# Optimization experiments

Hardware: AMD Instinct MI355X
Metric: run time of the kernel (lower is better)

## Reference

```python
import jax, jax.numpy as jnp
import numpy as np

N, CIN, T, V = 32, 64, 256, 25
COUT = 192
K = 3                      # num_subset
INTER = COUT // 4          # coff_embedding = 4 -> 48
MID = COUT // 3            # 64
EPS = 1e-5


def _bn(x, g, b):
    # training-mode BatchNorm2d over (N, T, V) per channel
    m = x.mean(axis=(0, 2, 3), keepdims=True)
    v = x.var(axis=(0, 2, 3), keepdims=True)
    return (x - m) * jax.lax.rsqrt(v + EPS) * g[None, :, None, None] + b[None, :, None, None]


def _conv1x1(x, w, b):
    # w: [O, C]
    return jnp.einsum('oc,nctv->notv', w, x) + b[None, :, None, None]


def _tconv(x, w, b, pad):
    # w: [O, C, k, 1] temporal conv along T
    y = jax.lax.conv_general_dilated(x, w, (1, 1), ((pad, pad), (0, 0)),
                                     dimension_numbers=('NCHW', 'OIHW', 'NCHW'))
    return y + b[None, :, None, None]


def setup_inputs() -> dict:
    key = jax.random.key(0)
    ks = jax.random.split(key, 24)
    r = lambda i, shape, s=0.05: jax.random.normal(ks[i], shape, jnp.float32) * s
    return {
        'x': r(0, (N, CIN, T, V), 1.0),
        'A': jax.random.uniform(ks[1], (K, V, V), jnp.float32),   # fixed adjacency buffer
        'PA': jnp.full((K, V, V), 1e-6, jnp.float32),
        'Wa': r(2, (K, INTER, CIN)), 'ba': jnp.zeros((K, INTER), jnp.float32),
        'Wb': r(3, (K, INTER, CIN)), 'bb': jnp.zeros((K, INTER), jnp.float32),
        'Wd': r(4, (K, COUT, CIN)), 'bd': jnp.zeros((K, COUT), jnp.float32),
        'gcn_bn_g': jnp.ones(COUT, jnp.float32), 'gcn_bn_b': jnp.zeros(COUT, jnp.float32),
        'down_w': r(5, (COUT, CIN)), 'down_b': jnp.zeros(COUT, jnp.float32),
        'down_bn_g': jnp.ones(COUT, jnp.float32), 'down_bn_b': jnp.zeros(COUT, jnp.float32),
        'W11': r(6, (COUT, COUT)), 'b11': jnp.zeros(COUT, jnp.float32),
        'W21': r(7, (COUT, COUT)), 'b21': jnp.zeros(COUT, jnp.float32),
        'W31': r(8, (COUT, COUT)), 'b31': jnp.zeros(COUT, jnp.float32),
        'W12': r(9, (MID, COUT, 1, 1)), 'b12': jnp.zeros(MID, jnp.float32),
        'W22': r(10, (MID, COUT, 3, 1)), 'b22': jnp.zeros(MID, jnp.float32),
        'W32': r(11, (MID, COUT, 7, 1)), 'b32': jnp.zeros(MID, jnp.float32),
        'tcn_bn_g': jnp.ones(COUT, jnp.float32), 'tcn_bn_b': jnp.zeros(COUT, jnp.float32),
        'res_w': r(12, (COUT, CIN)), 'res_b': jnp.zeros(COUT, jnp.float32),
        'res_bn_g': jnp.ones(COUT, jnp.float32), 'res_bn_b': jnp.zeros(COUT, jnp.float32),
    }


def reference(x, A, PA, Wa, ba, Wb, bb, Wd, bd, gcn_bn_g, gcn_bn_b,
              down_w, down_b, down_bn_g, down_bn_b,
              W11, b11, W21, b21, W31, b31, W12, b12, W22, b22, W32, b32,
              tcn_bn_g, tcn_bn_b, res_w, res_b, res_bn_g, res_bn_b):
    n, c, t, v = x.shape
    # ---- unit_gcn (all num_subset branches vectorized over axis k) ----
    fa = jnp.einsum('kic,nctv->nkitv', Wa, x) + ba[None, :, :, None, None]
    fb = jnp.einsum('kic,nctv->nkitv', Wb, x) + bb[None, :, :, None, None]
    A1 = fa.transpose(0, 1, 4, 2, 3).reshape(n, K, v, INTER * t)   # [n,k,V,inter*T]
    A2 = fb.reshape(n, K, INTER * t, v)                            # [n,k,inter*T,V]
    scores = jnp.einsum('nkvd,nkdw->nkvw', A1, A2) / A1.shape[-1]
    att = jax.nn.softmax(scores, axis=-2) + (A + PA)[None]         # softmax over rows (dim -2)
    xv = x.reshape(n, c * t, v)
    z = jnp.einsum('ndv,nkvw->nkdw', xv, att).reshape(n, K, c, t, v)
    y = jnp.einsum('koc,nkctv->notv', Wd, z) + bd.sum(axis=0)[None, :, None, None]
    y = _bn(y, gcn_bn_g, gcn_bn_b)
    y = y + _bn(_conv1x1(x, down_w, down_b), down_bn_g, down_bn_b)
    g = jax.nn.relu(y)
    # ---- unit_tcn_m: three parallel (1x1 conv -> temporal conv) branches ----
    x1 = _tconv(_conv1x1(g, W11, b11), W12, b12, 0)
    x2 = _tconv(_conv1x1(g, W21, b21), W22, b22, 1)
    x3 = _tconv(_conv1x1(g, W31, b31), W32, b32, 3)
    tm = _bn(jnp.concatenate([x1, x2, x3], axis=1), tcn_bn_g, tcn_bn_b)
    # ---- residual: 1x1 unit_tcn on original input ----
    res = _bn(_conv1x1(x, res_w, res_b), res_bn_g, res_bn_b)
    return jax.nn.relu(tm + res)
```

## Files before the change

kernel.cpp:

```cpp
#include <hip/hip_runtime.h>
#include <hip/hip_bf16.h>
#include <cstdint>
#include <cstddef>

#define EPS_  1e-5f
#define NTV_  204800

typedef unsigned short u16;
typedef __attribute__((ext_vector_type(8))) short short8;
typedef __attribute__((ext_vector_type(4))) float f32x4;

__device__ __forceinline__ float bf2f(u16 u) {
  uint32_t x = (uint32_t)u << 16;
  float f;
  __builtin_memcpy(&f, &x, 4);
  return f;
}
__device__ __forceinline__ u16 f2bf(float f) {
  uint32_t x;
  __builtin_memcpy(&x, &f, 4);
  uint32_t r = (x + 0x7FFFu + ((x >> 16) & 1u)) >> 16;
  return (u16)r;
}

__device__ __forceinline__ void gload_lds16(const u16* g, u16* l) {
  __builtin_amdgcn_global_load_lds(
      (const __attribute__((address_space(1))) uint32_t*)g,
      (__attribute__((address_space(3))) uint32_t*)l, 16, 0, 0);
}

__global__ __launch_bounds__(256) void k_cvtw(
    const float* __restrict__ Wa, const float* __restrict__ Wb_,
    const float* __restrict__ dw, const float* __restrict__ rw,
    const float* __restrict__ W11, const float* __restrict__ W21, const float* __restrict__ W31,
    const float* __restrict__ Wd, const float* __restrict__ W12, const float* __restrict__ W22,
    const float* __restrict__ W32, const float* __restrict__ bd,
    const float* __restrict__ ba, const float* __restrict__ bb,
    const float* __restrict__ downbi, const float* __restrict__ resbi,
    const float* __restrict__ b11, const float* __restrict__ b21, const float* __restrict__ b31,
    u16* __restrict__ WB, float* __restrict__ bd2, float* __restrict__ fbias,
    float* __restrict__ cbias)
{
  int i = blockIdx.x * 256 + threadIdx.x;
  if (i < 9216) { WB[i] = f2bf(Wa[i]); return; }
  i -= 9216;
  if (i < 9216) { WB[9216 + i] = f2bf(Wb_[i]); return; }
  i -= 9216;
  if (i < 12288) { WB[18432 + i] = f2bf(dw[i]); return; }
  i -= 12288;
  if (i < 12288) { WB[30720 + i] = f2bf(rw[i]); return; }
  i -= 12288;
  if (i < 36864) { WB[43008 + i] = f2bf(W11[i]); return; }
  i -= 36864;
  if (i < 36864) { WB[79872 + i] = f2bf(W21[i]); return; }
  i -= 36864;
  if (i < 36864) { WB[116736 + i] = f2bf(W31[i]); return; }
  i -= 36864;
  if (i < 36864) {
    const int o = i / 192, r = i % 192, k = r >> 6, c = r & 63;
    WB[153600 + i] = f2bf(Wd[((size_t)(k * 192 + o)) * 64 + c]);
    return;
  }
  i -= 36864;
  if (i < 12288) { WB[190464 + i] = f2bf(W12[i]); return; }
  i -= 12288;
  if (i < 36864) {
    const int tap = i / 12288, q = i % 12288, o = q / 192, c = q % 192;
    WB[202752 + i] = f2bf(W22[((size_t)(o * 192 + c)) * 3 + tap]);
    return;
  }
  i -= 36864;
  if (i < 86016) {
    const int tap = i / 12288, q = i % 12288, o = q / 192, c = q % 192;
    WB[239616 + i] = f2bf(W32[((size_t)(o * 192 + c)) * 7 + tap]);
    return;
  }
  i -= 86016;
  if (i < 192) { bd2[i] = bd[i] + bd[192 + i] + bd[384 + i]; return; }
  i -= 192;
  if (i < 288) { fbias[i] = (i < 144) ? ba[i] : bb[i - 144]; return; }
  i -= 288;
  if (i < 960) {
    const int g = i / 192, o = i % 192;
    float v;
    if (g == 0) v = downbi[o];
    else if (g == 1) v = resbi[o];
    else if (g == 2) v = b11[o];
    else if (g == 3) v = b21[o];
    else v = b31[o];
    cbias[i] = v;
  }
}

__global__ __launch_bounds__(256) void k_xpose(const float* __restrict__ x, u16* __restrict__ xb)
{
  __shared__ u16 xt[256][72];
  const int bx = blockIdx.x;
  const int n = bx / 25, s0 = (bx % 25) * 256;
  const int tid = threadIdx.x;
  for (int l = tid; l < 64 * 64; l += 256) {
    const int c = l >> 6, q = l & 63;
    float4 v = *(const float4*)&x[((size_t)n * 64 + c) * 6400 + s0 + q * 4];
    xt[q * 4 + 0][c] = f2bf(v.x);
    xt[q * 4 + 1][c] = f2bf(v.y);
    xt[q * 4 + 2][c] = f2bf(v.z);
    xt[q * 4 + 3][c] = f2bf(v.w);
  }
  __syncthreads();
  for (int l = tid; l < 256 * 8; l += 256) {
    const int row = l >> 3, seg = l & 7;
    const int s_old = s0 + row;
    const int dv = s_old % 25, dt = s_old / 25;
    *(uint4*)&xb[((size_t)n * 6400 + dv * 256 + dt) * 64 + seg * 8] = *(const uint4*)&xt[row][seg * 8];
  }
}

template<int C, int NP, bool STATS>
__global__ __launch_bounds__(192) void k_conv5(
    const u16* __restrict__ in, const u16* __restrict__ Wb,
    const float* __restrict__ bias,
    u16* __restrict__ out0, u16* __restrict__ out1, u16* __restrict__ out2,
    float* __restrict__ stSum, float* __restrict__ stSq)
{
  constexpr int CS = C / 8;
  constexpr int CH = C / 32;
  constexpr int SB = 128 * CS;
  __shared__ u16 Bt[128 * C];
  __shared__ u16 Ep[3][16 * 72];

  const int bx = blockIdx.x;
  const int nb = bx / 50;
  const int sb = (bx % 50) * 128;
  const int tid = threadIdx.x;
  const int w = tid >> 6, lane = tid & 63;
  const int lr = lane & 15, lg = lane >> 4;

  for (int base = 0; base < SB; base += 192) {
    const int slot = base + tid;
    if ((SB % 192 == 0) || slot < SB) {
      const int r = slot / CS, q = slot % CS;
      gload_lds16(&in[((size_t)nb * 6400 + sb + r) * C + ((q ^ (r & 7)) << 3)],
                  &Bt[(size_t)(base + w * 64) * 8]);
    }
  }
  __syncthreads();

  u16* sc = Ep[w];
  const int o_w = w * 64;
  const int s0 = lane >> 3, seg = lane & 7;

  for (int p = 0; p < NP; ++p) {
    u16* outp = (p == 0) ? out0 : ((p == 1) ? out1 : out2);
    const u16* Ap = Wb + (size_t)p * 192 * C;
    short8 af[4][CH];
#pragma unroll
    for (int mi = 0; mi < 4; ++mi)
#pragma unroll
      for (int j = 0; j < CH; ++j)
        af[mi][j] = *(const short8*)&Ap[((size_t)(o_w + mi * 16 + lr)) * C + j * 32 + lg * 8];
    float4 bv[4];
#pragma unroll
    for (int mi = 0; mi < 4; ++mi)
      bv[mi] = *(const float4*)&bias[p * 192 + o_w + mi * 16 + lg * 4];
    float ssum[4][4] = {}, ssq[4][4] = {};

#pragma unroll
    for (int t = 0; t < 8; ++t) {
      f32x4 acc[4];
#pragma unroll
      for (int mi = 0; mi < 4; ++mi) {
        acc[mi][0] = 0.f; acc[mi][1] = 0.f; acc[mi][2] = 0.f; acc[mi][3] = 0.f;
      }
      const int rr = t * 16 + lr;
#pragma unroll
      for (int j = 0; j < CH; ++j) {
        short8 bf = *(const short8*)&Bt[((size_t)rr * CS + ((j * 4 + lg) ^ (rr & 7))) * 8];
#pragma unroll
        for (int mi = 0; mi < 4; ++mi)
          acc[mi] = __builtin_amdgcn_mfma_f32_16x16x32_bf16(af[mi][j], bf, acc[mi], 0, 0, 0);
      }
#pragma unroll
      for (int mi = 0; mi < 4; ++mi)
#pragma unroll
        for (int r = 0; r < 4; ++r) {
          float vv = acc[mi][r] + ((const float*)&bv[mi])[r];
          if (STATS) { ssum[mi][r] += vv; ssq[mi][r] += vv * vv; }
          sc[lr * 72 + mi * 16 + lg * 4 + r] = f2bf(vv);
        }
#pragma unroll
      for (int pass = 0; pass < 2; ++pass) {
        const int s = pass * 8 + s0;
        uint4 val = *(const uint4*)&sc[s * 72 + seg * 8];
        *(uint4*)&outp[((size_t)nb * 6400 + sb + t * 16 + s) * 192 + o_w + seg * 8] = val;
      }
    }

    if (STATS) {
#pragma unroll
      for (int mi = 0; mi < 4; ++mi)
#pragma unroll
        for (int r = 0; r < 4; ++r) {
          float ss = ssum[mi][r], sq = ssq[mi][r];
#pragma unroll
          for (int m = 1; m < 16; m <<= 1) { ss += __shfl_xor(ss, m); sq += __shfl_xor(sq, m); }
          if (lr == 0) {
            const int og = p * 192 + o_w + mi * 16 + lg * 4 + r;
            const int slot = bx & 15;
            atomicAdd(&stSum[og * 16 + slot], ss);
            atomicAdd(&stSq[og * 16 + slot], sq);
          }
        }
    }
  }
}

template<int KT>
__global__ __launch_bounds__(256, 2) void k_tconv4(
    const u16* __restrict__ in, const u16* __restrict__ Wb,
    const float* __restrict__ bias, u16* __restrict__ out,
    float* __restrict__ stSum, float* __restrict__ stSq,
    const u16* __restrict__ zp, int o_off)
{
  constexpr int C = 192, CS = 24, CH = 6;
  constexpr int HALO = KT / 2;
  constexpr int BR = 128 + 2 * HALO;
  __shared__ u16 Bt[BR * C];
  __shared__ u16 Ep[4][16 * 24];

  const int bx = blockIdx.x;
  const int nb = bx / 50;
  const int sb = (bx % 50) * 128;
  const int tbase = sb & 255;
  const int tid = threadIdx.x;
  const int w = tid >> 6, lane = tid & 63;
  const int lr = lane & 15, lg = lane >> 4;

  constexpr int SB = BR * CS;
  for (int base = 0; base < SB; base += 256) {
    const int slot = base + tid;
    if ((SB % 256 == 0) || slot < SB) {
      const int r = slot / CS, q = slot % CS;
      const int t = tbase - HALO + r;
      const u16* src = (HALO == 0 || (unsigned)t < 256u)
          ? &in[((size_t)nb * 6400 + sb - HALO + r) * C + ((q ^ (r & 7)) << 3)]
          : zp;
      gload_lds16(src, &Bt[(size_t)(base + w * 64) * 8]);
    }
  }
  __syncthreads();

  f32x4 acc[8];
#pragma unroll
  for (int t = 0; t < 8; ++t) {
    acc[t][0] = 0.f; acc[t][1] = 0.f; acc[t][2] = 0.f; acc[t][3] = 0.f;
  }

  for (int tap = 0; tap < KT; ++tap) {
    short8 af[CH];
#pragma unroll
    for (int j = 0; j < CH; ++j)
      af[j] = *(const short8*)&Wb[((size_t)(tap * 64 + w * 16 + lr)) * C + j * 32 + lg * 8];
#pragma unroll
    for (int t = 0; t < 8; ++t) {
      const int rr = t * 16 + lr + tap;
#pragma unroll
      for (int j = 0; j < CH; ++j) {
        short8 bf = *(const short8*)&Bt[((size_t)rr * CS + ((j * 4 + lg) ^ (rr & 7))) * 8];
        acc[t] = __builtin_amdgcn_mfma_f32_16x16x32_bf16(af[j], bf, acc[t], 0, 0, 0);
      }
    }
  }

  const float4 bv4 = *(const float4*)&bias[w * 16 + lg * 4];
  const int row2 = lane >> 2, q2 = lane & 3;
  float ssum[4] = {}, ssq[4] = {};
#pragma unroll
  for (int t = 0; t < 8; ++t) {
    u16* sc = Ep[w];
#pragma unroll
    for (int r = 0; r < 4; ++r) {
      float vv = acc[t][r] + ((const float*)&bv4)[r];
      ssum[r] += vv; ssq[r] += vv * vv;
      sc[lr * 24 + lg * 4 + r] = f2bf(vv);
    }
    uint2 val = *(const uint2*)&sc[row2 * 24 + q2 * 4];
    *(uint2*)&out[((size_t)nb * 6400 + sb + t * 16 + row2) * 192 +
                  o_off + w * 16 + q2 * 4] = val;
  }
#pragma unroll
  for (int r = 0; r < 4; ++r) {
    float ss = ssum[r], sq = ssq[r];
#pragma unroll
    for (int m = 1; m < 16; m <<= 1) { ss += __shfl_xor(ss, m); sq += __shfl_xor(sq, m); }
    if (lr == 0) {
      const int og = o_off + w * 16 + lg * 4 + r;
      const int slot = bx & 15;
      atomicAdd(&stSum[og * 16 + slot], ss);
      atomicAdd(&stSq[og * 16 + slot], sq);
    }
  }
}

__global__ __launch_bounds__(256) void k_gemm_cf(
    const u16* __restrict__ in, const u16* __restrict__ Wb,
    const float* __restrict__ bias, u16* __restrict__ out)
{
  __shared__ u16 Bt[128 * 64];
  __shared__ u16 At[288 * 64];
  __shared__ u16 SC[48 * 136];

  const int bx = blockIdx.x;
  const int nb = bx / 50;
  const int sb = (bx % 50) * 128;
  const int v = sb >> 8, tbase = sb & 255;
  const int tid = threadIdx.x;
  const int w = tid >> 6, lane = tid & 63;
  const int lr = lane & 15, lg = lane >> 4;
  const int s_w = w * 32;

  for (int base = 0; base < 1024; base += 256) {
    const int slot = base + tid;
    const int r = slot >> 3, q = slot & 7;
    gload_lds16(&in[((size_t)nb * 6400 + v * 256 + tbase + r) * 64 + ((q ^ (r & 7)) << 3)],
                &Bt[(size_t)(base + w * 64) * 8]);
  }
  for (int base = 0; base < 2304; base += 256) {
    const int slot = base + tid;
    const int r = slot >> 3, q = slot & 7;
    gload_lds16(&Wb[(size_t)r * 64 + ((q ^ (r & 7)) << 3)],
                &At[(size_t)(base + w * 64) * 8]);
  }
  __syncthreads();

  for (int p = 0; p < 6; ++p) {
    f32x4 acc[3][2];
#pragma unroll
    for (int mi = 0; mi < 3; ++mi)
#pragma unroll
      for (int ni = 0; ni < 2; ++ni) {
        acc[mi][ni][0] = 0.f; acc[mi][ni][1] = 0.f; acc[mi][ni][2] = 0.f; acc[mi][ni][3] = 0.f;
      }
#pragma unroll
    for (int ch = 0; ch < 2; ++ch) {
      const int j = ch * 4 + lg;
      short8 af[3], bf[2];
#pragma unroll
      for (int mi = 0; mi < 3; ++mi) {
        const int r = p * 48 + mi * 16 + lr;
        af[mi] = *(const short8*)&At[((size_t)r * 8 + (j ^ (r & 7))) * 8];
      }
#pragma unroll
      for (int ni = 0; ni < 2; ++ni) {
        const int r = s_w + ni * 16 + lr;
        bf[ni] = *(const short8*)&Bt[((size_t)r * 8 + (j ^ (r & 7))) * 8];
      }
#pragma unroll
      for (int mi = 0; mi < 3; ++mi)
#pragma unroll
        for (int ni = 0; ni < 2; ++ni)
          acc[mi][ni] = __builtin_amdgcn_mfma_f32_16x16x32_bf16(af[mi], bf[ni], acc[mi][ni], 0, 0, 0);
    }
#pragma unroll
    for (int mi = 0; mi < 3; ++mi)
#pragma unroll
      for (int r = 0; r < 4; ++r) {
        const float bv = bias[p * 48 + mi * 16 + lg * 4 + r];
#pragma unroll
        for (int ni = 0; ni < 2; ++ni) acc[mi][ni][r] += bv;
      }
    __syncthreads();
#pragma unroll
    for (int mi = 0; mi < 3; ++mi)
#pragma unroll
      for (int ni = 0; ni < 2; ++ni)
#pragma unroll
        for (int r = 0; r < 4; ++r)
          SC[(mi * 16 + lg * 4 + r) * 136 + s_w + ni * 16 + lr] = f2bf(acc[mi][ni][r]);
    __syncthreads();
#pragma unroll
    for (int it = 0; it < 3; ++it) {
      const int row = it * 16 + (tid >> 4), chunk = tid & 15;
      *(uint4*)&out[((size_t)nb * 288 + p * 48 + row) * 6400 + sb + chunk * 8] =
          *(const uint4*)&SC[row * 136 + chunk * 8];
    }
  }
}

__device__ __forceinline__ float dot4(uint2 a, uint2 b) {
  return bf2f((u16)(a.x & 0xffff)) * bf2f((u16)(b.x & 0xffff)) +
         bf2f((u16)(a.x >> 16))    * bf2f((u16)(b.x >> 16)) +
         bf2f((u16)(a.y & 0xffff)) * bf2f((u16)(b.y & 0xffff)) +
         bf2f((u16)(a.y >> 16))    * bf2f((u16)(b.y >> 16));
}

__global__ __launch_bounds__(256) void k_scores_part(
    const u16* __restrict__ fab, float* __restrict__ part)
{
  const int nk = blockIdx.x;
  const int seg = blockIdx.y;
  const int n = nk / 3, k = nk % 3;
  __shared__ u16 sa[12800], sb[12800];
  const int tid = threadIdx.x;
  const u16* fap = fab + ((size_t)(n * 288 + k * 48 + seg * 2)) * 6400;
  const u16* fbp = fab + ((size_t)(n * 288 + 144 + k * 48 + seg * 2)) * 6400;
  for (int l = tid; l < 1600; l += 256) {
    ((uint4*)sa)[l] = ((const uint4*)fap)[l];
    ((uint4*)sb)[l] = ((const uint4*)fbp)[l];
  }
  __syncthreads();

  const int l0 = tid, l1 = tid + 256, l2 = tid + 512;
  const bool ok2 = (l2 < 625);
  const int v0 = l0 / 25, w0 = l0 % 25;
  const int v1 = l1 / 25, w1 = l1 % 25;
  const int v2 = ok2 ? l2 / 25 : 0, w2 = ok2 ? l2 % 25 : 0;
  float a0 = 0.f, a1 = 0.f, a2 = 0.f;
  const int rot = ((tid & 63) * 4) & 255;

#pragma unroll
  for (int ch = 0; ch < 2; ++ch) {
    const u16* pa = sa + ch * 6400;
    const u16* pb = sb + ch * 6400;
    for (int it = 0; it < 64; ++it) {
      const int t = (it * 4 + rot) & 255;
      a0 += dot4(*(const uint2*)&pa[v0 * 256 + t], *(const uint2*)&pb[w0 * 256 + t]);
      a1 += dot4(*(const uint2*)&pa[v1 * 256 + t], *(const uint2*)&pb[w1 * 256 + t]);
      if (ok2)
        a2 += dot4(*(const uint2*)&pa[v2 * 256 + t], *(const uint2*)&pb[w2 * 256 + t]);
    }
  }
  float* po = part + ((size_t)nk * 24 + seg) * 640;
  po[l0] = a0;
  po[l1] = a1;
  if (ok2) po[l2] = a2;
}

__global__ __launch_bounds__(256) void k_softmax(
    const float* __restrict__ part, const float* __restrict__ A,
    const float* __restrict__ PA, float* __restrict__ att)
{
  const int nk = blockIdx.x;
  const int n = nk / 3, k = nk % 3;
  __shared__ float sc[640];
  const int tid = threadIdx.x;
  const float* pb = part + (size_t)nk * 24 * 640;
  for (int l = tid; l < 625; l += 256) {
    float s = 0.f;
#pragma unroll
    for (int seg = 0; seg < 24; ++seg) s += pb[seg * 640 + l];
    sc[l] = s;
  }
  __syncthreads();
  if (tid < 25) {
    const int w = tid;
    const float scale = 1.f / 12288.f;
    float m = -1e30f;
    for (int v = 0; v < 25; ++v) m = fmaxf(m, sc[v * 25 + w]);
    m *= scale;
    float e[25], sum = 0.f;
#pragma unroll
    for (int v = 0; v < 25; ++v) { e[v] = __expf(sc[v * 25 + w] * scale - m); sum += e[v]; }
    const float inv = 1.f / sum;
    const float* Ak = A + k * 625;
    const float* Pk = PA + k * 625;
    float* ao = att + ((size_t)n * 3 + k) * 625;
#pragma unroll
    for (int v = 0; v < 25; ++v) ao[v * 25 + w] = e[v] * inv + Ak[v * 25 + w] + Pk[v * 25 + w];
  }
}

__global__ __launch_bounds__(256) void k_z(
    const u16* __restrict__ xb, const float* __restrict__ att, u16* __restrict__ z)
{
  __shared__ float attl[1950];
  __shared__ u16 xt[12800];
  const int bx = blockIdx.x;
  const int n = bx >> 5, tb = (bx & 31) * 8;
  const int tid = threadIdx.x;

  for (int l = tid; l < 1875; l += 256) {
    const int k = l / 625, vw = l % 625, v = vw / 25, w = vw % 25;
    attl[(k * 25 + v) * 26 + w] = att[((size_t)n * 3 + k) * 625 + vw];
  }
  for (int l = tid; l < 200 * 8; l += 256) {
    const int j = l >> 3, seg = l & 7;
    const int vv = j >> 3, tl = j & 7;
    *(uint4*)&xt[j * 64 + seg * 8] =
        *(const uint4*)&xb[((size_t)n * 6400 + vv * 256 + tb + tl) * 64 + seg * 8];
  }
  __syncthreads();

  for (int it = 0; it < 19; ++it) {
    const int l = tid + it * 256;
    if (l >= 4800) break;
    const int hi = l >> 6, lo = l & 63;
    const int k = hi / 25, w = hi % 25;
    const int tl = lo >> 3, c0 = (lo & 7) * 8;
    float accv[8] = {};
    for (int v = 0; v < 25; ++v) {
      const float aw = attl[(k * 25 + v) * 26 + w];
      union { uint4 u; u16 s[8]; } xv;
      xv.u = *(const uint4*)&xt[(v * 8 + tl) * 64 + c0];
#pragma unroll
      for (int jj = 0; jj < 8; ++jj) accv[jj] += aw * bf2f(xv.s[jj]);
    }
    union { uint4 u; u16 s[8]; } ov;
#pragma unroll
    for (int jj = 0; jj < 8; ++jj) ov.s[jj] = f2bf(accv[jj]);
    *(uint4*)&z[((size_t)n * 6400 + w * 256 + tb + tl) * 192 + k * 64 + c0] = ov.u;
  }
}

__global__ void k_bnparams(const float* __restrict__ sSum, const float* __restrict__ sSq,
                           const float* __restrict__ gamma, const float* __restrict__ beta,
                           float* __restrict__ a, float* __restrict__ c, int O)
{
  const int o = threadIdx.x + blockIdx.x * blockDim.x;
  if (o >= O) return;
  float sum = 0.f, sq = 0.f;
#pragma unroll
  for (int s = 0; s < 16; ++s) { sum += sSum[o * 16 + s]; sq += sSq[o * 16 + s]; }
  const float mean = sum * (1.f / NTV_);
  const float var = sq * (1.f / NTV_) - mean * mean;
  const float inv = rsqrtf(var + EPS_);
  const float av = gamma[o] * inv;
  a[o] = av;
  c[o] = beta[o] - av * mean;
}

__global__ __launch_bounds__(256) void k_g2(
    const u16* __restrict__ ypre, const u16* __restrict__ down,
    const float* __restrict__ ga, const float* __restrict__ gc,
    const float* __restrict__ da, const float* __restrict__ dc,
    u16* __restrict__ g)
{
  __shared__ float pA1[192], pC1[192], pA2[192], pC2[192];
  const int tid = threadIdx.x;
  if (tid < 192) { pA1[tid] = ga[tid]; pC1[tid] = gc[tid]; pA2[tid] = da[tid]; pC2[tid] = dc[tid]; }
  __syncthreads();
  for (size_t i8 = (size_t)blockIdx.x * 256 + tid; i8 < 4915200; i8 += (size_t)gridDim.x * 256) {
    const int c0 = (int)(i8 % 24) * 8;
    union { uint4 u; u16 s[8]; } yv, dv, ov;
    yv.u = *(const uint4*)&ypre[i8 * 8];
    dv.u = *(const uint4*)&down[i8 * 8];
#pragma unroll
    for (int j = 0; j < 8; ++j) {
      const int c = c0 + j;
      ov.s[j] = f2bf(fmaxf(pA1[c] * bf2f(yv.s[j]) + pC1[c] + pA2[c] * bf2f(dv.s[j]) + pC2[c], 0.f));
    }
    *(uint4*)&g[i8 * 8] = ov.u;
  }
}

__global__ __launch_bounds__(256) void k_out(
    const u16* __restrict__ tm, const u16* __restrict__ resp,
    const float* __restrict__ ta, const float* __restrict__ tc,
    const float* __restrict__ ra, const float* __restrict__ rc,
    float* __restrict__ out)
{
  __shared__ u16 L[100][200];
  __shared__ float pA1[192], pC1[192], pA2[192], pC2[192];
  const int bx = blockIdx.x;
  const int n = bx >> 6, t0 = (bx & 63) * 4;
  const int tid = threadIdx.x;
  if (tid < 192) { pA1[tid] = ta[tid]; pC1[tid] = tc[tid]; pA2[tid] = ra[tid]; pC2[tid] = rc[tid]; }
  __syncthreads();
  for (int l = tid; l < 2400; l += 256) {
    const int row = l / 24, ch = l % 24;
    const int v = row >> 2, tl = row & 3;
    const size_t src = ((size_t)n * 6400 + v * 256 + t0 + tl) * 192 + ch * 8;
    union { uint4 u; u16 s[8]; } tv, rv;
    tv.u = *(const uint4*)&tm[src];
    rv.u = *(const uint4*)&resp[src];
#pragma unroll
    for (int j = 0; j < 8; ++j) {
      const int c = ch * 8 + j;
      L[row][c] = f2bf(fmaxf(pA1[c] * bf2f(tv.s[j]) + pC1[c] + pA2[c] * bf2f(rv.s[j]) + pC2[c], 0.f));
    }
  }
  __syncthreads();
  for (int j = tid; j < 192 * 25; j += 256) {
    const int o = j / 25, q = j % 25;
    float4 f4;
#pragma unroll
    for (int e = 0; e < 4; ++e) {
      const int idx = q * 4 + e;
      const int tl = idx / 25, v = idx % 25;
      ((float*)&f4)[e] = bf2f(L[v * 4 + tl][o]);
    }
    *(float4*)&out[((size_t)n * 192 + o) * 6400 + t0 * 25 + q * 4] = f4;
  }
}

extern "C" void kernel_launch(void* const* d_in, const int* in_sizes, int n_in,
                              void* d_out, int out_size, void* d_ws, size_t ws_size,
                              hipStream_t stream)
{
  const float* x      = (const float*)d_in[0];
  const float* A      = (const float*)d_in[1];
  const float* PA     = (const float*)d_in[2];
  const float* Wa     = (const float*)d_in[3];
  const float* ba     = (const float*)d_in[4];
  const float* Wb     = (const float*)d_in[5];
  const float* bb     = (const float*)d_in[6];
  const float* Wd     = (const float*)d_in[7];
  const float* bd     = (const float*)d_in[8];
  const float* gcng   = (const float*)d_in[9];
  const float* gcnb   = (const float*)d_in[10];
  const float* downw  = (const float*)d_in[11];
  const float* downbi = (const float*)d_in[12];
  const float* downg  = (const float*)d_in[13];
  const float* downb  = (const float*)d_in[14];
  const float* W11    = (const float*)d_in[15];
  const float* b11    = (const float*)d_in[16];
  const float* W21    = (const float*)d_in[17];
  const float* b21    = (const float*)d_in[18];
  const float* W31    = (const float*)d_in[19];
  const float* b31    = (const float*)d_in[20];
  const float* W12    = (const float*)d_in[21];
  const float* b12    = (const float*)d_in[22];
  const float* W22    = (const float*)d_in[23];
  const float* b22    = (const float*)d_in[24];
  const float* W32    = (const float*)d_in[25];
  const float* b32    = (const float*)d_in[26];
  const float* tcng   = (const float*)d_in[27];
  const float* tcnb   = (const float*)d_in[28];
  const float* resw   = (const float*)d_in[29];
  const float* resbi  = (const float*)d_in[30];
  const float* resg   = (const float*)d_in[31];
  const float* resb   = (const float*)d_in[32];
  (void)in_sizes; (void)n_in; (void)out_size; (void)ws_size;

  u16* ob = (u16*)d_out;
  u16* fab   = ob;
  u16* xb    = ob + 58982400;
  float* att = (float*)(ob + 72089600);
  float* part  = (float*)(ob + 72584768);
  float* fbias = (float*)(ob + 75533888);
  u16* btmp2 = ob;
  u16* btmp3 = ob + 39321600;

  char* ws = (char*)d_ws;
  const size_t SLOT = 78643200;
  u16* z     = (u16*)(ws);
  u16* g     = (u16*)(ws);
  u16* ypre  = (u16*)(ws + SLOT);
  u16* btmp1 = (u16*)(ws + SLOT);
  u16* down  = (u16*)(ws + 2 * SLOT);
  u16* tm    = (u16*)(ws + 2 * SLOT);
  u16* resp  = (u16*)(ws + 3 * SLOT);
  char* sm   = ws + 4 * SLOT;
  float* bnp   = (float*)(sm);
  u16*   zp    = (u16*)(sm + 8192);
  u16*   WB    = (u16*)(sm + 8704);
  float* bd2   = (float*)(sm + 660224);
  float* cbias = (float*)(sm + 661248);
  float* slots = (float*)(sm + 665600);
  float* gcnSum = slots;           float* gcnSq = slots + 3072;
  float* dwnSum = slots + 6144;    float* resSum = slots + 9216;
  float* dwnSq  = slots + 12288;   float* resSq  = slots + 15360;
  float* tmSum  = slots + 18432;   float* tmSq   = slots + 21504;
  float* gcnA = bnp;          float* gcnC = bnp + 192;
  float* dwnA = bnp + 384;    float* dwnC = bnp + 576;
  float* resA = bnp + 768;    float* resC = bnp + 960;
  float* tmA  = bnp + 1152;   float* tmC  = bnp + 1344;

  hipMemsetAsync(slots, 0, 24576 * 4, stream);
  hipMemsetAsync(zp, 0, 256, stream);

  const dim3 blk(256);
  const dim3 blk3(192);

  k_cvtw<<<dim3(1278), blk, 0, stream>>>(Wa, Wb, downw, resw, W11, W21, W31,
                                         Wd, W12, W22, W32, bd, ba, bb,
                                         downbi, resbi, b11, b21, b31,
                                         WB, bd2, fbias, cbias);
  k_xpose<<<dim3(800), blk, 0, stream>>>(x, xb);

  k_gemm_cf<<<dim3(1600), blk, 0, stream>>>(xb, WB, fbias, fab);
  k_scores_part<<<dim3(96, 24), blk, 0, stream>>>(fab, part);
  k_softmax<<<dim3(96), blk, 0, stream>>>(part, A, PA, att);
  k_z<<<dim3(1024), blk, 0, stream>>>(xb, att, z);
  k_conv5<192, 1, true><<<dim3(1600), blk3, 0, stream>>>(
      z, WB + 153600, bd2, ypre, ypre, ypre, gcnSum, gcnSq);
  k_conv5<64, 2, true><<<dim3(1600), blk3, 0, stream>>>(
      xb, WB + 18432, cbias, down, resp, resp, dwnSum, dwnSq);
  k_bnparams<<<dim3(1), dim3(192), 0, stream>>>(gcnSum, gcnSq, gcng, gcnb, gcnA, gcnC, 192);
  k_bnparams<<<dim3(1), dim3(192), 0, stream>>>(dwnSum, dwnSq, downg, downb, dwnA, dwnC, 192);
  k_bnparams<<<dim3(1), dim3(192), 0, stream>>>(resSum, resSq, resg, resb, resA, resC, 192);
  k_g2<<<dim3(2048), blk, 0, stream>>>(ypre, down, gcnA, gcnC, dwnA, dwnC, g);

  k_conv5<192, 3, false><<<dim3(1600), blk3, 0, stream>>>(
      g, WB + 43008, cbias + 384, btmp1, btmp2, btmp3, nullptr, nullptr);
  k_tconv4<1><<<dim3(1600), blk, 0, stream>>>(
      btmp1, WB + 190464, b12, tm, tmSum, tmSq, zp, 0);
  k_tconv4<3><<<dim3(1600), blk, 0, stream>>>(
      btmp2, WB + 202752, b22, tm, tmSum, tmSq, zp, 64);
  k_tconv4<7><<<dim3(1600), blk, 0, stream>>>(
      btmp3, WB + 239616, b32, tm, tmSum, tmSq, zp, 128);
  k_bnparams<<<dim3(1), dim3(192), 0, stream>>>(tmSum, tmSq, tcng, tcnb, tmA, tmC, 192);

  k_out<<<dim3(2048), blk, 0, stream>>>(tm, resp, tmA, tmC, resA, resC, (float*)d_out);
}
```

Before: 923.7 us.

## Halve conv tiles, widen blocks, and merge three temporal convs into one launch

The 1x1 conv kernel now handles 64 positions per block with 384 threads (6 waves, each owning 32 output channels) instead of 128 positions with 3 waves. Its epilogue stages a full 64x192 bf16 tile in LDS and writes whole rows with coalesced 16-byte stores. The three temporal-conv branches become a single launch with blockIdx.y selecting the branch, using a runtime tap count, a shared 3-row halo and 64-row tiles. The aim is more blocks, higher occupancy, fewer launches and better-coalesced output stores. The cost is more halo reloading per output row, less weight reuse per block, and a runtime loop bound in the tconv kernel.

```diff
diff --git a/kernel.cpp b/kernel.cpp
--- a/kernel.cpp
+++ b/kernel.cpp
@@ -116,7 +116,7 @@
 }
 
 template<int C, int NP, bool STATS>
-__global__ __launch_bounds__(192) void k_conv5(
+__global__ __launch_bounds__(384) void k_conv6(
     const u16* __restrict__ in, const u16* __restrict__ Wb,
     const float* __restrict__ bias,
     u16* __restrict__ out0, u16* __restrict__ out1, u16* __restrict__ out2,
@@ -124,20 +124,20 @@
 {
   constexpr int CS = C / 8;
   constexpr int CH = C / 32;
-  constexpr int SB = 128 * CS;
-  __shared__ u16 Bt[128 * C];
-  __shared__ u16 Ep[3][16 * 72];
+  constexpr int SB = 64 * CS;
+  __shared__ u16 Bt[64 * C];
+  __shared__ u16 Ep[64][200];
 
   const int bx = blockIdx.x;
-  const int nb = bx / 50;
-  const int sb = (bx % 50) * 128;
+  const int nb = bx / 100;
+  const int sb = (bx % 100) * 64;
   const int tid = threadIdx.x;
   const int w = tid >> 6, lane = tid & 63;
   const int lr = lane & 15, lg = lane >> 4;
 
-  for (int base = 0; base < SB; base += 192) {
+  for (int base = 0; base < SB; base += 384) {
     const int slot = base + tid;
-    if ((SB % 192 == 0) || slot < SB) {
+    if ((SB % 384 == 0) || slot < SB) {
       const int r = slot / CS, q = slot % CS;
       gload_lds16(&in[((size_t)nb * 6400 + sb + r) * C + ((q ^ (r & 7)) << 3)],
                   &Bt[(size_t)(base + w * 64) * 8]);
@@ -145,30 +145,30 @@
   }
   __syncthreads();
 
-  u16* sc = Ep[w];
-  const int o_w = w * 64;
-  const int s0 = lane >> 3, seg = lane & 7;
+  const int oc = w * 32;
 
   for (int p = 0; p < NP; ++p) {
     u16* outp = (p == 0) ? out0 : ((p == 1) ? out1 : out2);
     const u16* Ap = Wb + (size_t)p * 192 * C;
-    short8 af[4][CH];
-#pragma unroll
-    for (int mi = 0; mi < 4; ++mi)
+    short8 af[2][CH];
+#pragma unroll
+    for (int mi = 0; mi < 2; ++mi)
 #pragma unroll
       for (int j = 0; j < CH; ++j)
-        af[mi][j] = *(const short8*)&Ap[((size_t)(o_w + mi * 16 + lr)) * C + j * 32 + lg * 8];
-    float4 bv[4];
-#pragma unroll
-    for (int mi = 0; mi < 4; ++mi)
-      bv[mi] = *(const float4*)&bias[p * 192 + o_w + mi * 16 + lg * 4];
-    float ssum[4][4] = {}, ssq[4][4] = {};
-
-#pragma unroll
-    for (int t = 0; t < 8; ++t) {
-      f32x4 acc[4];
-#pragma unroll
-      for (int mi = 0; mi < 4; ++mi) {
+        af[mi][j] = *(const short8*)&Ap[((size_t)(oc + mi * 16 + lr)) * C + j * 32 + lg * 8];
+    float4 bv[2];
+#pragma unroll
+    for (int mi = 0; mi < 2; ++mi)
+      bv[mi] = *(const float4*)&bias[p * 192 + oc + mi * 16 + lg * 4];
+    float ssum[2][4] = {}, ssq[2][4] = {};
+
+    if (p) __syncthreads();
+
+#pragma unroll
+    for (int t = 0; t < 4; ++t) {
+      f32x4 acc[2];
+#pragma unroll
+      for (int mi = 0; mi < 2; ++mi) {
         acc[mi][0] = 0.f; acc[mi][1] = 0.f; acc[mi][2] = 0.f; acc[mi][3] = 0.f;
       }
       const int rr = t * 16 + lr;
@@ -176,35 +176,40 @@
       for (int j = 0; j < CH; ++j) {
         short8 bf = *(const short8*)&Bt[((size_t)rr * CS + ((j * 4 + lg) ^ (rr & 7))) * 8];
 #pragma unroll
-        for (int mi = 0; mi < 4; ++mi)
+        for (int mi = 0; mi < 2; ++mi)
           acc[mi] = __builtin_amdgcn_mfma_f32_16x16x32_bf16(af[mi][j], bf, acc[mi], 0, 0, 0);
       }
 #pragma unroll
-      for (int mi = 0; mi < 4; ++mi)
+      for (int mi = 0; mi < 2; ++mi) {
+        union { uint2 u; u16 s[4]; } pk;
 #pragma unroll
         for (int r = 0; r < 4; ++r) {
           float vv = acc[mi][r] + ((const float*)&bv[mi])[r];
           if (STATS) { ssum[mi][r] += vv; ssq[mi][r] += vv * vv; }
-          sc[lr * 72 + mi * 16 + lg * 4 + r] = f2bf(vv);
+          pk.s[r] = f2bf(vv);
         }
-#pragma unroll
-      for (int pass = 0; pass < 2; ++pass) {
-        const int s = pass * 8 + s0;
-        uint4 val = *(const uint4*)&sc[s * 72 + seg * 8];
-        *(uint4*)&outp[((size_t)nb * 6400 + sb + t * 16 + s) * 192 + o_w + seg * 8] = val;
+        *(uint2*)&Ep[rr][oc + mi * 16 + lg * 4] = pk.u;
       }
     }
+    __syncthreads();
+
+#pragma unroll
+    for (int pass = 0; pass < 4; ++pass) {
+      const int idx = pass * 384 + tid;
+      const int row = idx / 24, ch = idx % 24;
+      *(uint4*)&outp[((size_t)nb * 6400 + sb + row) * 192 + ch * 8] = *(const uint4*)&Ep[row][ch * 8];
+    }
 
     if (STATS) {
 #pragma unroll
-      for (int mi = 0; mi < 4; ++mi)
+      for (int mi = 0; mi < 2; ++mi)
 #pragma unroll
         for (int r = 0; r < 4; ++r) {
           float ss = ssum[mi][r], sq = ssq[mi][r];
 #pragma unroll
           for (int m = 1; m < 16; m <<= 1) { ss += __shfl_xor(ss, m); sq += __shfl_xor(sq, m); }
           if (lr == 0) {
-            const int og = p * 192 + o_w + mi * 16 + lg * 4 + r;
+            const int og = p * 192 + oc + mi * 16 + lg * 4 + r;
             const int slot = bx & 15;
             atomicAdd(&stSum[og * 16 + slot], ss);
             atomicAdd(&stSq[og * 16 + slot], sq);
@@ -214,22 +219,27 @@
   }
 }
 
-template<int KT>
-__global__ __launch_bounds__(256, 2) void k_tconv4(
-    const u16* __restrict__ in, const u16* __restrict__ Wb,
-    const float* __restrict__ bias, u16* __restrict__ out,
-    float* __restrict__ stSum, float* __restrict__ stSq,
-    const u16* __restrict__ zp, int o_off)
+__global__ __launch_bounds__(256) void k_tconv6(
+    const u16* __restrict__ b1, const u16* __restrict__ b2, const u16* __restrict__ b3,
+    const u16* __restrict__ WB,
+    const float* __restrict__ bias12, const float* __restrict__ bias22, const float* __restrict__ bias32,
+    u16* __restrict__ out, float* __restrict__ stSum, float* __restrict__ stSq,
+    const u16* __restrict__ zp)
 {
   constexpr int C = 192, CS = 24, CH = 6;
-  constexpr int HALO = KT / 2;
-  constexpr int BR = 128 + 2 * HALO;
+  constexpr int BR = 64 + 6;
   __shared__ u16 Bt[BR * C];
-  __shared__ u16 Ep[4][16 * 24];
+  __shared__ u16 Ep[64][72];
+
+  const int br = blockIdx.y;
+  const u16* in = (br == 0) ? b1 : ((br == 1) ? b2 : b3);
+  const float* bias = (br == 0) ? bias12 : ((br == 1) ? bias22 : bias32);
+  const int KT = (br == 0) ? 1 : ((br == 1) ? 3 : 7);
+  const u16* Wp = WB + ((br == 0) ? 190464 : ((br == 1) ? 202752 : 239616));
 
   const int bx = blockIdx.x;
-  const int nb = bx / 50;
-  const int sb = (bx % 50) * 128;
+  const int nb = bx / 100;
+  const int sb = (bx % 100) * 64;
   const int tbase = sb & 255;
   const int tid = threadIdx.x;
   const int w = tid >> 6, lane = tid & 63;
@@ -238,31 +248,32 @@
   constexpr int SB = BR * CS;
   for (int base = 0; base < SB; base += 256) {
     const int slot = base + tid;
-    if ((SB % 256 == 0) || slot < SB) {
+    if (slot < SB) {
       const int r = slot / CS, q = slot % CS;
-      const int t = tbase - HALO + r;
-      const u16* src = (HALO == 0 || (unsigned)t < 256u)
-          ? &in[((size_t)nb * 6400 + sb - HALO + r) * C + ((q ^ (r & 7)) << 3)]
+      const int t = tbase - 3 + r;
+      const u16* src = ((unsigned)t < 256u)
+          ? &in[((size_t)nb * 6400 + sb - 3 + r) * C + ((q ^ (r & 7)) << 3)]
           : zp;
       gload_lds16(src, &Bt[(size_t)(base + w * 64) * 8]);
     }
   }
   __syncthreads();
 
-  f32x4 acc[8];
-#pragma unroll
-  for (int t = 0; t < 8; ++t) {
+  f32x4 acc[4];
+#pragma unroll
+  for (int t = 0; t < 4; ++t) {
     acc[t][0] = 0.f; acc[t][1] = 0.f; acc[t][2] = 0.f; acc[t][3] = 0.f;
   }
 
+  const int hofs = 3 - KT / 2;
   for (int tap = 0; tap < KT; ++tap) {
     short8 af[CH];
 #pragma unroll
     for (int j = 0; j < CH; ++j)
-      af[j] = *(const short8*)&Wb[((size_t)(tap * 64 + w * 16 + lr)) * C + j * 32 + lg * 8];
-#pragma unroll
-    for (int t = 0; t < 8; ++t) {
-      const int rr = t * 16 + lr + tap;
+      af[j] = *(const short8*)&Wp[((size_t)(tap * 64 + w * 16 + lr)) * C + j * 32 + lg * 8];
+#pragma unroll
+    for (int t = 0; t < 4; ++t) {
+      const int rr = t * 16 + lr + hofs + tap;
 #pragma unroll
       for (int j = 0; j < CH; ++j) {
         short8 bf = *(const short8*)&Bt[((size_t)rr * CS + ((j * 4 + lg) ^ (rr & 7))) * 8];
@@ -272,28 +283,35 @@
   }
 
   const float4 bv4 = *(const float4*)&bias[w * 16 + lg * 4];
-  const int row2 = lane >> 2, q2 = lane & 3;
   float ssum[4] = {}, ssq[4] = {};
 #pragma unroll
-  for (int t = 0; t < 8; ++t) {
-    u16* sc = Ep[w];
+  for (int t = 0; t < 4; ++t) {
+    union { uint2 u; u16 s[4]; } pk;
 #pragma unroll
     for (int r = 0; r < 4; ++r) {
       float vv = acc[t][r] + ((const float*)&bv4)[r];
       ssum[r] += vv; ssq[r] += vv * vv;
-      sc[lr * 24 + lg * 4 + r] = f2bf(vv);
-    }
-    uint2 val = *(const uint2*)&sc[row2 * 24 + q2 * 4];
-    *(uint2*)&out[((size_t)nb * 6400 + sb + t * 16 + row2) * 192 +
-                  o_off + w * 16 + q2 * 4] = val;
-  }
+      pk.s[r] = f2bf(vv);
+    }
+    *(uint2*)&Ep[t * 16 + lr][w * 16 + lg * 4] = pk.u;
+  }
+  __syncthreads();
+
+#pragma unroll
+  for (int pass = 0; pass < 2; ++pass) {
+    const int idx = pass * 256 + tid;
+    const int row = idx >> 3, ch = idx & 7;
+    *(uint4*)&out[((size_t)nb * 6400 + sb + row) * 192 + br * 64 + ch * 8] =
+        *(const uint4*)&Ep[row][ch * 8];
+  }
+
 #pragma unroll
   for (int r = 0; r < 4; ++r) {
     float ss = ssum[r], sq = ssq[r];
 #pragma unroll
     for (int m = 1; m < 16; m <<= 1) { ss += __shfl_xor(ss, m); sq += __shfl_xor(sq, m); }
     if (lr == 0) {
-      const int og = o_off + w * 16 + lg * 4 + r;
+      const int og = br * 64 + w * 16 + lg * 4 + r;
       const int slot = bx & 15;
       atomicAdd(&stSum[og * 16 + slot], ss);
       atomicAdd(&stSq[og * 16 + slot], sq);
@@ -669,7 +687,7 @@
   hipMemsetAsync(zp, 0, 256, stream);
 
   const dim3 blk(256);
-  const dim3 blk3(192);
+  const dim3 blk6(384);
 
   k_cvtw<<<dim3(1278), blk, 0, stream>>>(Wa, Wb, downw, resw, W11, W21, W31,
                                          Wd, W12, W22, W32, bd, ba, bb,
@@ -681,23 +699,19 @@
   k_scores_part<<<dim3(96, 24), blk, 0, stream>>>(fab, part);
   k_softmax<<<dim3(96), blk, 0, stream>>>(part, A, PA, att);
   k_z<<<dim3(1024), blk, 0, stream>>>(xb, att, z);
-  k_conv5<192, 1, true><<<dim3(1600), blk3, 0, stream>>>(
+  k_conv6<192, 1, true><<<dim3(3200), blk6, 0, stream>>>(
       z, WB + 153600, bd2, ypre, ypre, ypre, gcnSum, gcnSq);
-  k_conv5<64, 2, true><<<dim3(1600), blk3, 0, stream>>>(
+  k_conv6<64, 2, true><<<dim3(3200), blk6, 0, stream>>>(
       xb, WB + 18432, cbias, down, resp, resp, dwnSum, dwnSq);
   k_bnparams<<<dim3(1), dim3(192), 0, stream>>>(gcnSum, gcnSq, gcng, gcnb, gcnA, gcnC, 192);
   k_bnparams<<<dim3(1), dim3(192), 0, stream>>>(dwnSum, dwnSq, downg, downb, dwnA, dwnC, 192);
   k_bnparams<<<dim3(1), dim3(192), 0, stream>>>(resSum, resSq, resg, resb, resA, resC, 192);
   k_g2<<<dim3(2048), blk, 0, stream>>>(ypre, down, gcnA, gcnC, dwnA, dwnC, g);
 
-  k_conv5<192, 3, false><<<dim3(1600), blk3, 0, stream>>>(
+  k_conv6<192, 3, false><<<dim3(3200), blk6, 0, stream>>>(
       g, WB + 43008, cbias + 384, btmp1, btmp2, btmp3, nullptr, nullptr);
-  k_tconv4<1><<<dim3(1600), blk, 0, stream>>>(
-      btmp1, WB + 190464, b12, tm, tmSum, tmSq, zp, 0);
-  k_tconv4<3><<<dim3(1600), blk, 0, stream>>>(
-      btmp2, WB + 202752, b22, tm, tmSum, tmSq, zp, 64);
-  k_tconv4<7><<<dim3(1600), blk, 0, stream>>>(
-      btmp3, WB + 239616, b32, tm, tmSum, tmSq, zp, 128);
+  k_tconv6<<<dim3(3200, 3), blk, 0, stream>>>(
+      btmp1, btmp2, btmp3, WB, b12, b22, b32, tm, tmSum, tmSq, zp);
   k_bnparams<<<dim3(1), dim3(192), 0, stream>>>(tmSum, tmSq, tcng, tcnb, tmA, tmC, 192);
 
   k_out<<<dim3(2048), blk, 0, stream>>>(tm, resp, tmA, tmC, resA, resC, (float*)d_out);
```

After: 1.029 ms. 1.11x slower.

## Fuse three temporal-conv branches into one kernel with full-row coalesced stores

Applied to the files above, without the earlier changes.

Replaces three separate templated temporal-conv launches with a single kernel in which each block processes all three branches (kernel sizes 1, 3 and 7) for a 64-row tile. Outputs are staged in shared memory so each block writes complete 192-channel rows with 16-byte stores, instead of scattered 8-byte partial-row writes. This removes two launches and improves output write coalescing. In exchange, KT becomes a runtime value so the tap loop is no longer specialized, halo loads are always sized for 7 taps, tiles are smaller, and the larger LDS footprint may lower occupancy.

```diff
diff --git a/kernel.cpp b/kernel.cpp
--- a/kernel.cpp
+++ b/kernel.cpp
@@ -214,90 +214,102 @@
   }
 }
 
-template<int KT>
-__global__ __launch_bounds__(256, 2) void k_tconv4(
-    const u16* __restrict__ in, const u16* __restrict__ Wb,
-    const float* __restrict__ bias, u16* __restrict__ out,
-    float* __restrict__ stSum, float* __restrict__ stSq,
-    const u16* __restrict__ zp, int o_off)
+__global__ __launch_bounds__(256) void k_tconv7(
+    const u16* __restrict__ b1, const u16* __restrict__ b2, const u16* __restrict__ b3,
+    const u16* __restrict__ WB,
+    const float* __restrict__ bias12, const float* __restrict__ bias22, const float* __restrict__ bias32,
+    u16* __restrict__ out, float* __restrict__ stSum, float* __restrict__ stSq,
+    const u16* __restrict__ zp)
 {
   constexpr int C = 192, CS = 24, CH = 6;
-  constexpr int HALO = KT / 2;
-  constexpr int BR = 128 + 2 * HALO;
+  constexpr int BR = 70;
   __shared__ u16 Bt[BR * C];
-  __shared__ u16 Ep[4][16 * 24];
+  __shared__ u16 Ep[64][200];
 
   const int bx = blockIdx.x;
-  const int nb = bx / 50;
-  const int sb = (bx % 50) * 128;
+  const int nb = bx / 100;
+  const int sb = (bx % 100) * 64;
   const int tbase = sb & 255;
   const int tid = threadIdx.x;
   const int w = tid >> 6, lane = tid & 63;
   const int lr = lane & 15, lg = lane >> 4;
 
-  constexpr int SB = BR * CS;
-  for (int base = 0; base < SB; base += 256) {
-    const int slot = base + tid;
-    if ((SB % 256 == 0) || slot < SB) {
-      const int r = slot / CS, q = slot % CS;
-      const int t = tbase - HALO + r;
-      const u16* src = (HALO == 0 || (unsigned)t < 256u)
-          ? &in[((size_t)nb * 6400 + sb - HALO + r) * C + ((q ^ (r & 7)) << 3)]
-          : zp;
-      gload_lds16(src, &Bt[(size_t)(base + w * 64) * 8]);
-    }
-  }
-  __syncthreads();
-
-  f32x4 acc[8];
-#pragma unroll
-  for (int t = 0; t < 8; ++t) {
-    acc[t][0] = 0.f; acc[t][1] = 0.f; acc[t][2] = 0.f; acc[t][3] = 0.f;
-  }
-
-  for (int tap = 0; tap < KT; ++tap) {
-    short8 af[CH];
-#pragma unroll
-    for (int j = 0; j < CH; ++j)
-      af[j] = *(const short8*)&Wb[((size_t)(tap * 64 + w * 16 + lr)) * C + j * 32 + lg * 8];
-#pragma unroll
-    for (int t = 0; t < 8; ++t) {
-      const int rr = t * 16 + lr + tap;
-#pragma unroll
-      for (int j = 0; j < CH; ++j) {
-        short8 bf = *(const short8*)&Bt[((size_t)rr * CS + ((j * 4 + lg) ^ (rr & 7))) * 8];
-        acc[t] = __builtin_amdgcn_mfma_f32_16x16x32_bf16(af[j], bf, acc[t], 0, 0, 0);
-      }
-    }
-  }
-
-  const float4 bv4 = *(const float4*)&bias[w * 16 + lg * 4];
-  const int row2 = lane >> 2, q2 = lane & 3;
-  float ssum[4] = {}, ssq[4] = {};
-#pragma unroll
-  for (int t = 0; t < 8; ++t) {
-    u16* sc = Ep[w];
+  for (int br = 0; br < 3; ++br) {
+    const u16* in = (br == 0) ? b1 : ((br == 1) ? b2 : b3);
+    const float* bias = (br == 0) ? bias12 : ((br == 1) ? bias22 : bias32);
+    const int KT = (br == 0) ? 1 : ((br == 1) ? 3 : 7);
+    const u16* Wp = WB + ((br == 0) ? 190464 : ((br == 1) ? 202752 : 239616));
+
+    if (br) __syncthreads();
+    constexpr int SB = BR * CS;
+    for (int base = 0; base < SB; base += 256) {
+      const int slot = base + tid;
+      if (slot < SB) {
+        const int r = slot / CS, q = slot % CS;
+        const int t = tbase - 3 + r;
+        const u16* src = ((unsigned)t < 256u)
+            ? &in[((size_t)nb * 6400 + sb - 3 + r) * C + ((q ^ (r & 7)) << 3)]
+            : zp;
+        gload_lds16(src, &Bt[(size_t)(base + w * 64) * 8]);
+      }
+    }
+    __syncthreads();
+
+    f32x4 acc[4];
+#pragma unroll
+    for (int t = 0; t < 4; ++t) {
+      acc[t][0] = 0.f; acc[t][1] = 0.f; acc[t][2] = 0.f; acc[t][3] = 0.f;
+    }
+    const int hofs = 3 - KT / 2;
+    for (int tap = 0; tap < KT; ++tap) {
+      short8 af[CH];
+#pragma unroll
+      for (int j = 0; j < CH; ++j)
+        af[j] = *(const short8*)&Wp[((size_t)(tap * 64 + w * 16 + lr)) * C + j * 32 + lg * 8];
+#pragma unroll
+      for (int t = 0; t < 4; ++t) {
+        const int rr = t * 16 + lr + hofs + tap;
+#pragma unroll
+        for (int j = 0; j < CH; ++j) {
+          short8 bf = *(const short8*)&Bt[((size_t)rr * CS + ((j * 4 + lg) ^ (rr & 7))) * 8];
+          acc[t] = __builtin_amdgcn_mfma_f32_16x16x32_bf16(af[j], bf, acc[t], 0, 0, 0);
+        }
+      }
+    }
+
+    const float4 bv4 = *(const float4*)&bias[w * 16 + lg * 4];
+    float ssum[4] = {}, ssq[4] = {};
+#pragma unroll
+    for (int t = 0; t < 4; ++t) {
+      union { uint2 u; u16 s[4]; } pk;
+#pragma unroll
+      for (int r = 0; r < 4; ++r) {
+        float vv = acc[t][r] + ((const float*)&bv4)[r];
+        ssum[r] += vv; ssq[r] += vv * vv;
+        pk.s[r] = f2bf(vv);
+      }
+      *(uint2*)&Ep[t * 16 + lr][br * 64 + w * 16 + lg * 4] = pk.u;
+    }
 #pragma unroll
     for (int r = 0; r < 4; ++r) {
-      float vv = acc[t][r] + ((const float*)&bv4)[r];
-      ssum[r] += vv; ssq[r] += vv * vv;
-      sc[lr * 24 + lg * 4 + r] = f2bf(vv);
-    }
-    uint2 val = *(const uint2*)&sc[row2 * 24 + q2 * 4];
-    *(uint2*)&out[((size_t)nb * 6400 + sb + t * 16 + row2) * 192 +
-                  o_off + w * 16 + q2 * 4] = val;
-  }
-#pragma unroll
-  for (int r = 0; r < 4; ++r) {
-    float ss = ssum[r], sq = ssq[r];
-#pragma unroll
-    for (int m = 1; m < 16; m <<= 1) { ss += __shfl_xor(ss, m); sq += __shfl_xor(sq, m); }
-    if (lr == 0) {
-      const int og = o_off + w * 16 + lg * 4 + r;
-      const int slot = bx & 15;
-      atomicAdd(&stSum[og * 16 + slot], ss);
-      atomicAdd(&stSq[og * 16 + slot], sq);
-    }
+      float ss = ssum[r], sq = ssq[r];
+#pragma unroll
+      for (int m = 1; m < 16; m <<= 1) { ss += __shfl_xor(ss, m); sq += __shfl_xor(sq, m); }
+      if (lr == 0) {
+        const int og = br * 64 + w * 16 + lg * 4 + r;
+        const int slot = bx & 15;
+        atomicAdd(&stSum[og * 16 + slot], ss);
+        atomicAdd(&stSq[og * 16 + slot], sq);
+      }
+    }
+  }
+  __syncthreads();
+
+#pragma unroll
+  for (int pass = 0; pass < 6; ++pass) {
+    const int idx = pass * 256 + tid;
+    const int row = idx / 24, ch = idx % 24;
+    *(uint4*)&out[((size_t)nb * 6400 + sb + row) * 192 + ch * 8] = *(const uint4*)&Ep[row][ch * 8];
   }
 }
 
@@ -692,12 +704,8 @@
 
   k_conv5<192, 3, false><<<dim3(1600), blk3, 0, stream>>>(
       g, WB + 43008, cbias + 384, btmp1, btmp2, btmp3, nullptr, nullptr);
-  k_tconv4<1><<<dim3(1600), blk, 0, stream>>>(
-      btmp1, WB + 190464, b12, tm, tmSum, tmSq, zp, 0);
-  k_tconv4<3><<<dim3(1600), blk, 0, stream>>>(
-      btmp2, WB + 202752, b22, tm, tmSum, tmSq, zp, 64);
-  k_tconv4<7><<<dim3(1600), blk, 0, stream>>>(
-      btmp3, WB + 239616, b32, tm, tmSum, tmSq, zp, 128);
+  k_tconv7<<<dim3(3200), blk, 0, stream>>>(
+      btmp1, btmp2, btmp3, WB, b12, b22, b32, tm, tmSum, tmSq, zp);
   k_bnparams<<<dim3(1), dim3(192), 0, stream>>>(tmSum, tmSq, tcng, tcnb, tmA, tmC, 192);
 
   k_out<<<dim3(2048), blk, 0, stream>>>(tm, resp, tmA, tmC, resA, resC, (float*)d_out);
```

Measured after the change: 946.8 us. +2.5%, slower.
